# Performance work log

Measured on AMD Instinct MI355X. Metric: run time of the kernel, lower is better.

## Reference

```python
import jax, jax.numpy as jnp
import numpy as np

INPUT_SIZE = 512   # num_embeddings == RNN input feature dim
SEQ = INPUT_SIZE // 4   # 128, embedding dim == RNN seq_len
HID = 12
OUT = 3
B = 2048


def setup_inputs() -> dict:
    key = jax.random.key(0)
    ks = jax.random.split(key, 12)
    s = 0.1
    x = jax.random.randint(ks[0], (B, INPUT_SIZE), 0, INPUT_SIZE)
    emb = jax.random.normal(ks[1], (INPUT_SIZE, SEQ), dtype=jnp.float32) * s
    w_ih_f = jax.random.normal(ks[2], (HID, INPUT_SIZE), dtype=jnp.float32) * s
    w_hh_f = jax.random.normal(ks[3], (HID, HID), dtype=jnp.float32) * s
    b_ih_f = jax.random.normal(ks[4], (HID,), dtype=jnp.float32) * s
    b_hh_f = jax.random.normal(ks[5], (HID,), dtype=jnp.float32) * s
    w_ih_r = jax.random.normal(ks[6], (HID, INPUT_SIZE), dtype=jnp.float32) * s
    w_hh_r = jax.random.normal(ks[7], (HID, HID), dtype=jnp.float32) * s
    b_ih_r = jax.random.normal(ks[8], (HID,), dtype=jnp.float32) * s
    b_hh_r = jax.random.normal(ks[9], (HID,), dtype=jnp.float32) * s
    fc_w = jax.random.normal(ks[10], (OUT, 2 * HID), dtype=jnp.float32) * s
    fc_b = jax.random.normal(ks[11], (OUT,), dtype=jnp.float32) * s
    return {"x": x, "emb": emb,
            "w_ih_f": w_ih_f, "w_hh_f": w_hh_f, "b_ih_f": b_ih_f, "b_hh_f": b_hh_f,
            "w_ih_r": w_ih_r, "w_hh_r": w_hh_r, "b_ih_r": b_ih_r, "b_hh_r": b_hh_r,
            "fc_w": fc_w, "fc_b": fc_b}


def reference(x, emb, w_ih_f, w_hh_f, b_ih_f, b_hh_f,
              w_ih_r, w_hh_r, b_ih_r, b_hh_r, fc_w, fc_b):
    # embedding lookup: (B, INPUT_SIZE) -> (B, INPUT_SIZE, SEQ)
    e = emb[x]
    # view(-1, input_size, seq) is a no-op on this contiguous shape; swapaxes(1,2)
    xs = jnp.swapaxes(e, 1, 2)  # (B, SEQ, INPUT_SIZE): seq_len=SEQ, feat=INPUT_SIZE

    # forward-direction tanh RNN: precompute input projections, scan the recurrence
    pre = jnp.einsum('bsi,hi->sbh', xs, w_ih_f) + b_ih_f  # (SEQ, B, HID)

    def step(h, p):
        h = jnp.tanh(p + h @ w_hh_f.T + b_hh_f)
        return h, None

    h0 = jnp.zeros((xs.shape[0], HID), dtype=xs.dtype)
    h_fwd, _ = jax.lax.scan(step, h0, pre)  # final forward hidden (B, HID)

    # reverse-direction output at the LAST timestep = one step from zero hidden
    # on x_{T-1} (only out[:, -1, :] is consumed by the module)
    h_bwd = jnp.tanh(xs[:, -1, :] @ w_ih_r.T + b_ih_r + b_hh_r)  # (B, HID)

    out_last = jnp.concatenate([h_fwd, h_bwd], axis=-1)  # (B, 2*HID)
    return out_last @ fc_w.T + fc_b  # (B, OUT)
```

## Files before the change

### kernel.cpp

```cpp
#include <hip/hip_runtime.h>
#include <hip/hip_bf16.h>

#define B_N     2048
#define IN_N    512
#define SEQ_N   128
#define HID_N   12
#define HP_N    16
#define OUT_N   3

typedef __attribute__((ext_vector_type(8))) short short8;
typedef __attribute__((ext_vector_type(4))) float f32x4;
typedef unsigned int uint;
typedef unsigned short ushort;

__device__ __forceinline__ float fast_tanh(float x) {
    float e = __builtin_amdgcn_exp2f(x * 2.8853900817779268f);
    return 1.0f - 2.0f * __builtin_amdgcn_rcpf(e + 1.0f);
}

__device__ __forceinline__ ushort f2bf(float f) {
    uint u = __float_as_uint(f);
    u += 0x7fffu + ((u >> 16) & 1u);
    return (ushort)(u >> 16);
}

__device__ __forceinline__ float bf2f(ushort s) {
    return __uint_as_float(((uint)s) << 16);
}

__global__ __launch_bounds__(256) void k_prep(
    const float* __restrict__ emb, const float* __restrict__ w_ih_f,
    const float* __restrict__ w_ih_r,
    ushort* __restrict__ embB, ushort* __restrict__ wP)
{
    int tid = blockIdx.x * 256 + threadIdx.x;
    float4 e = ((const float4*)emb)[tid];
    uint2 o;
    o.x = (uint)f2bf(e.x) | ((uint)f2bf(e.y) << 16);
    o.y = (uint)f2bf(e.z) | ((uint)f2bf(e.w) << 16);
    ((uint2*)embB)[tid] = o;

    int j   = tid & 7;
    int l   = (tid >> 3) & 63;
    int src = (tid >> 9) & 1;
    int cks = tid >> 10;
    int h   = l & 15;
    int i   = (cks >> 2) * 128 + (cks & 3) * 32 + (l >> 4) * 8 + j;
    const float* wsrc = src ? w_ih_r : w_ih_f;
    wP[(((size_t)cks * 2 + src) * 64 + l) * 8 + j] =
        (h < HID_N) ? f2bf(wsrc[h * IN_N + i]) : (ushort)0;
}

__global__ __launch_bounds__(256, 2) void k_pre(
    const int* __restrict__ x, const ushort* __restrict__ embB,
    const ushort* __restrict__ wP,
    const float* __restrict__ b_ih_r, const float* __restrict__ b_hh_r,
    ushort* __restrict__ preB, float* __restrict__ rev)
{
    __shared__ __align__(16) ushort As[128 * 128];
    __shared__ __align__(16) ushort wPs[16384];

    const int t      = threadIdx.x;
    const int l      = t & 63;
    const int w      = t >> 6;
    const int lane16 = l & 15;
    const int quad   = l >> 4;
    const int il     = w * 32 + quad * 8;
    const int wg     = w * 4 + quad;
    const int l7     = lane16 & 7;
    const int so     = lane16 * 8;
    const int b0     = blockIdx.x * 4;

    {
        const uint4* s4 = (const uint4*)wP;
        uint4*       d4 = (uint4*)wPs;
        #pragma unroll
        for (int i = 0; i < 8; ++i) d4[t + i * 256] = s4[t + i * 256];
    }

    f32x4 acc0 = {0.f,0.f,0.f,0.f};
    f32x4 acc1 = {0.f,0.f,0.f,0.f};
    f32x4 accR = {0.f,0.f,0.f,0.f};
    uint R[8][4];

#define LD8(k, ix) { uint4 v = *(const uint4*)(embB + (size_t)(ix) * SEQ_N + so); \
        R[k][0]=v.x; R[k][1]=v.y; R[k][2]=v.z; R[k][3]=v.w; }

    int4 nA, nB;
    {
        const int* xq = x + (size_t)b0 * IN_N + il;
        nA = *(const int4*)xq;
        nB = *(const int4*)(xq + 4);
    }
    LD8(0, nA.x) LD8(1, nA.y) LD8(2, nA.z) LD8(3, nA.w)
    LD8(4, nB.x) LD8(5, nB.y) LD8(6, nB.z) LD8(7, nB.w)
    {
        const int* xq = x + (size_t)b0 * IN_N + 128 + il;
        nA = *(const int4*)xq;
        nB = *(const int4*)(xq + 4);
    }

    for (int p = 0; p < 16; ++p) {
        const int c = p & 3;

        #pragma unroll
        for (int pp = 0; pp < 8; ++pp) {
            const uint sel = (pp & 1) ? 0x07060302u : 0x05040100u;
            const int pv = pp >> 1;
            uint u0 = __builtin_amdgcn_perm(R[1][pv], R[0][pv], sel);
            uint u1 = __builtin_amdgcn_perm(R[3][pv], R[2][pv], sel);
            uint u2 = __builtin_amdgcn_perm(R[5][pv], R[4][pv], sel);
            uint u3 = __builtin_amdgcn_perm(R[7][pv], R[6][pv], sel);
            const int s    = lane16 * 8 + pp;
            const int slot = wg ^ pp ^ l7;
            *(uint4*)&As[(size_t)s * 128 + (size_t)slot * 8] =
                make_uint4(u0, u1, u2, u3);
        }

        if (p < 15) {
            LD8(0, nA.x) LD8(1, nA.y) LD8(2, nA.z) LD8(3, nA.w)
            LD8(4, nB.x) LD8(5, nB.y) LD8(6, nB.z) LD8(7, nB.w)
            if (p < 14) {
                const int pn = p + 2;
                const int* xq = x + (size_t)(b0 + (pn >> 2)) * IN_N
                                  + (pn & 3) * 128 + il;
                nA = *(const int4*)xq;
                nB = *(const int4*)(xq + 4);
            }
        }

        asm volatile("s_waitcnt lgkmcnt(0)" ::: "memory");
        __builtin_amdgcn_s_barrier();
        __builtin_amdgcn_sched_barrier(0);

        short8 bfr[4], bfrR[4];
        #pragma unroll
        for (int ks = 0; ks < 4; ++ks) {
            const ushort* wp = wPs + (size_t)((c * 4 + ks) * 128 + l) * 8;
            bfr[ks]  = *(const short8*)wp;
            bfrR[ks] = *(const short8*)(wp + 512);
        }

        #pragma unroll
        for (int tt = 0; tt < 2; ++tt) {
            const int row = (w * 2 + tt) * 16 + lane16;
            const int fr  = (row & 7) ^ ((row >> 3) & 7);
            #pragma unroll
            for (int ks = 0; ks < 4; ++ks) {
                const int slot = (ks * 4 + quad) ^ fr;
                short8 af = *(const short8*)&As[(size_t)row * 128 + (size_t)slot * 8];
                if (tt == 0) {
                    acc0 = __builtin_amdgcn_mfma_f32_16x16x32_bf16(af, bfr[ks], acc0, 0, 0, 0);
                } else {
                    acc1 = __builtin_amdgcn_mfma_f32_16x16x32_bf16(af, bfr[ks], acc1, 0, 0, 0);
                    accR = __builtin_amdgcn_mfma_f32_16x16x32_bf16(af, bfrR[ks], accR, 0, 0, 0);
                }
            }
        }

        if (c == 3) {
            const int bcur = b0 + (p >> 2);
            if (lane16 < HID_N) {
                #pragma unroll
                for (int r = 0; r < 4; ++r) {
                    const int s0v = (w * 2 + 0) * 16 + quad * 4 + r;
                    preB[((size_t)bcur * SEQ_N + s0v) * HP_N + lane16] = f2bf(acc0[r]);
                    const int s1v = (w * 2 + 1) * 16 + quad * 4 + r;
                    preB[((size_t)bcur * SEQ_N + s1v) * HP_N + lane16] = f2bf(acc1[r]);
                }
                if (w == 3 && quad == 3)
                    rev[bcur * HP_N + lane16] =
                        fast_tanh(accR[3] + b_ih_r[lane16] + b_hh_r[lane16]);
            }
            acc0 = (f32x4){0.f,0.f,0.f,0.f};
            acc1 = (f32x4){0.f,0.f,0.f,0.f};
            accR = (f32x4){0.f,0.f,0.f,0.f};
        }

        asm volatile("" ::: "memory");
        __builtin_amdgcn_s_barrier();
        __builtin_amdgcn_sched_barrier(0);
    }
#undef LD8
}

__global__ __launch_bounds__(256) void k_rnn(
    const ushort* __restrict__ preB, const float* __restrict__ rev,
    const float* __restrict__ w_hh_f,
    const float* __restrict__ b_ih_f, const float* __restrict__ b_hh_f,
    const float* __restrict__ fc_w, const float* __restrict__ fc_b,
    float* __restrict__ out)
{
    __shared__ float ho[16][40];

    const int tid = threadIdx.x;
    const int l   = tid & 63;
    const int j   = l & 15;
    const int jj  = (j < 12) ? j : 0;
    const int gid = tid >> 4;
    const int b   = blockIdx.x * 16 + gid;
    const int baseaddr = (l & 48) << 2;

    const float4* wr = (const float4*)(w_hh_f + jj * 12);
    float4 w0 = wr[0], w1 = wr[1], w2 = wr[2];
    float W[12] = {w0.x, w0.y, w0.z, w0.w, w1.x, w1.y, w1.z, w1.w,
                   w2.x, w2.y, w2.z, w2.w};
    const float bias = b_ih_f[jj] + b_hh_f[jj];

    const ushort* pb = preB + (size_t)b * SEQ_N * HP_N + j;
    ushort pq[8];
    #pragma unroll
    for (int k = 0; k < 8; ++k) pq[k] = pb[k * HP_N];

    float h = 0.f;
    for (int s8 = 0; s8 < 16; ++s8) {
        #pragma unroll
        for (int k = 0; k < 8; ++k) {
            int s = s8 * 8 + k;
            float p = bf2f(pq[k]) + bias;
            pq[k] = pb[((s + 8) & 127) * HP_N];
            int hb = __float_as_int(h);
            float hk[12];
            #pragma unroll
            for (int kk = 0; kk < 12; ++kk)
                hk[kk] = __int_as_float(__builtin_amdgcn_ds_bpermute(baseaddr + 4 * kk, hb));
            float c0 = p, c1 = 0.f, c2 = 0.f;
            #pragma unroll
            for (int u = 0; u < 4; ++u) {
                c0 = __builtin_fmaf(W[u],     hk[u],     c0);
                c1 = __builtin_fmaf(W[4 + u], hk[4 + u], c1);
                c2 = __builtin_fmaf(W[8 + u], hk[8 + u], c2);
            }
            h = fast_tanh(c0 + c1 + c2);
        }
    }

    ho[gid][j]      = h;
    ho[gid][20 + j] = rev[b * HP_N + j];
    if (j < OUT_N) {
        const float* fw = fc_w + j * 24;
        float o = fc_b[j];
        #pragma unroll
        for (int k = 0; k < 12; ++k)
            o += fw[k] * ho[gid][k] + fw[12 + k] * ho[gid][20 + k];
        out[b * OUT_N + j] = o;
    }
}

extern "C" void kernel_launch(void* const* d_in, const int* in_sizes, int n_in,
                              void* d_out, int out_size, void* d_ws, size_t ws_size,
                              hipStream_t stream) {
    const int*   x      = (const int*)  d_in[0];
    const float* emb    = (const float*)d_in[1];
    const float* w_ih_f = (const float*)d_in[2];
    const float* w_hh_f = (const float*)d_in[3];
    const float* b_ih_f = (const float*)d_in[4];
    const float* b_hh_f = (const float*)d_in[5];
    const float* w_ih_r = (const float*)d_in[6];
    const float* b_ih_r = (const float*)d_in[8];
    const float* b_hh_r = (const float*)d_in[9];
    const float* fc_w   = (const float*)d_in[10];
    const float* fc_b   = (const float*)d_in[11];
    float* out = (float*)d_out;

    ushort* preB = (ushort*)d_ws;
    float*  rev  = (float*)((char*)d_ws + 8388608);
    ushort* embB = (ushort*)((char*)d_ws + 8519680);
    ushort* wP   = (ushort*)((char*)d_ws + 8650752);

    k_prep<<<64,    256, 0, stream>>>(emb, w_ih_f, w_ih_r, embB, wP);
    k_pre <<<B_N/4, 256, 0, stream>>>(x, embB, wP, b_ih_r, b_hh_r, preB, rev);
    k_rnn <<<B_N/16,256, 0, stream>>>(preB, rev, w_hh_f, b_ih_f, b_hh_f, fc_w, fc_b, out);
}
```

Before: 117.6 us.

## Reorder projection loop by chunk with double-buffered gathers; two sequences per RNN thread

The projection kernel now loops over feature chunks in the outer loop and the four batch rows in the inner loop. It keeps four sets of accumulators and two register buffers for embedding gathers, so weight fragments are loaded once per chunk and the gathers run further ahead. The recurrence kernel now has each thread process two batch rows at once, interleaving two independent dependency chains to hide bpermute and tanh latency. The grid is halved to 64 blocks. This costs more registers and reduces the number of blocks in the latency-bound RNN stage.

```diff
diff --git a/kernel.cpp b/kernel.cpp
--- a/kernel.cpp
+++ b/kernel.cpp
@@ -78,110 +78,130 @@
         for (int i = 0; i < 8; ++i) d4[t + i * 256] = s4[t + i * 256];
     }
 
-    f32x4 acc0 = {0.f,0.f,0.f,0.f};
-    f32x4 acc1 = {0.f,0.f,0.f,0.f};
-    f32x4 accR = {0.f,0.f,0.f,0.f};
-    uint R[8][4];
-
-#define LD8(k, ix) { uint4 v = *(const uint4*)(embB + (size_t)(ix) * SEQ_N + so); \
-        R[k][0]=v.x; R[k][1]=v.y; R[k][2]=v.z; R[k][3]=v.w; }
-
-    int4 nA, nB;
-    {
-        const int* xq = x + (size_t)b0 * IN_N + il;
-        nA = *(const int4*)xq;
-        nB = *(const int4*)(xq + 4);
-    }
-    LD8(0, nA.x) LD8(1, nA.y) LD8(2, nA.z) LD8(3, nA.w)
-    LD8(4, nB.x) LD8(5, nB.y) LD8(6, nB.z) LD8(7, nB.w)
-    {
-        const int* xq = x + (size_t)b0 * IN_N + 128 + il;
-        nA = *(const int4*)xq;
-        nB = *(const int4*)(xq + 4);
-    }
-
-    for (int p = 0; p < 16; ++p) {
-        const int c = p & 3;
-
-        #pragma unroll
-        for (int pp = 0; pp < 8; ++pp) {
-            const uint sel = (pp & 1) ? 0x07060302u : 0x05040100u;
-            const int pv = pp >> 1;
-            uint u0 = __builtin_amdgcn_perm(R[1][pv], R[0][pv], sel);
-            uint u1 = __builtin_amdgcn_perm(R[3][pv], R[2][pv], sel);
-            uint u2 = __builtin_amdgcn_perm(R[5][pv], R[4][pv], sel);
-            uint u3 = __builtin_amdgcn_perm(R[7][pv], R[6][pv], sel);
-            const int s    = lane16 * 8 + pp;
-            const int slot = wg ^ pp ^ l7;
-            *(uint4*)&As[(size_t)s * 128 + (size_t)slot * 8] =
-                make_uint4(u0, u1, u2, u3);
-        }
-
-        if (p < 15) {
-            LD8(0, nA.x) LD8(1, nA.y) LD8(2, nA.z) LD8(3, nA.w)
-            LD8(4, nB.x) LD8(5, nB.y) LD8(6, nB.z) LD8(7, nB.w)
-            if (p < 14) {
-                const int pn = p + 2;
-                const int* xq = x + (size_t)(b0 + (pn >> 2)) * IN_N
-                                  + (pn & 3) * 128 + il;
-                nA = *(const int4*)xq;
-                nB = *(const int4*)(xq + 4);
-            }
-        }
-
-        asm volatile("s_waitcnt lgkmcnt(0)" ::: "memory");
-        __builtin_amdgcn_s_barrier();
-        __builtin_amdgcn_sched_barrier(0);
-
+    f32x4 a0_0={0.f,0.f,0.f,0.f}, a0_1={0.f,0.f,0.f,0.f}, a0_2={0.f,0.f,0.f,0.f}, a0_3={0.f,0.f,0.f,0.f};
+    f32x4 a1_0={0.f,0.f,0.f,0.f}, a1_1={0.f,0.f,0.f,0.f}, a1_2={0.f,0.f,0.f,0.f}, a1_3={0.f,0.f,0.f,0.f};
+    f32x4 aR_0={0.f,0.f,0.f,0.f}, aR_1={0.f,0.f,0.f,0.f}, aR_2={0.f,0.f,0.f,0.f}, aR_3={0.f,0.f,0.f,0.f};
+
+    uint RA[8][4], RB[8][4];
+    int4 IA0, IA1, IB0, IB1;
+
+#define IDXLD(Ilo, Ihi, bq2, c2) do { \
+    const int* xq_ = x + (size_t)(b0 + (bq2)) * IN_N + (c2) * 128 + il; \
+    Ilo = *(const int4*)xq_;  Ihi = *(const int4*)(xq_ + 4); \
+} while (0)
+
+#define GFETCH(Rb, Ilo, Ihi) do { uint4 v_; \
+    v_ = *(const uint4*)(embB + (size_t)(Ilo).x * SEQ_N + so); Rb[0][0]=v_.x; Rb[0][1]=v_.y; Rb[0][2]=v_.z; Rb[0][3]=v_.w; \
+    v_ = *(const uint4*)(embB + (size_t)(Ilo).y * SEQ_N + so); Rb[1][0]=v_.x; Rb[1][1]=v_.y; Rb[1][2]=v_.z; Rb[1][3]=v_.w; \
+    v_ = *(const uint4*)(embB + (size_t)(Ilo).z * SEQ_N + so); Rb[2][0]=v_.x; Rb[2][1]=v_.y; Rb[2][2]=v_.z; Rb[2][3]=v_.w; \
+    v_ = *(const uint4*)(embB + (size_t)(Ilo).w * SEQ_N + so); Rb[3][0]=v_.x; Rb[3][1]=v_.y; Rb[3][2]=v_.z; Rb[3][3]=v_.w; \
+    v_ = *(const uint4*)(embB + (size_t)(Ihi).x * SEQ_N + so); Rb[4][0]=v_.x; Rb[4][1]=v_.y; Rb[4][2]=v_.z; Rb[4][3]=v_.w; \
+    v_ = *(const uint4*)(embB + (size_t)(Ihi).y * SEQ_N + so); Rb[5][0]=v_.x; Rb[5][1]=v_.y; Rb[5][2]=v_.z; Rb[5][3]=v_.w; \
+    v_ = *(const uint4*)(embB + (size_t)(Ihi).z * SEQ_N + so); Rb[6][0]=v_.x; Rb[6][1]=v_.y; Rb[6][2]=v_.z; Rb[6][3]=v_.w; \
+    v_ = *(const uint4*)(embB + (size_t)(Ihi).w * SEQ_N + so); Rb[7][0]=v_.x; Rb[7][1]=v_.y; Rb[7][2]=v_.z; Rb[7][3]=v_.w; \
+} while (0)
+
+#define PACKR(Rb) do { \
+    _Pragma("unroll") \
+    for (int pp = 0; pp < 8; ++pp) { \
+        const uint sel_ = (pp & 1) ? 0x07060302u : 0x05040100u; \
+        const int pv_ = pp >> 1; \
+        uint u0_ = __builtin_amdgcn_perm(Rb[1][pv_], Rb[0][pv_], sel_); \
+        uint u1_ = __builtin_amdgcn_perm(Rb[3][pv_], Rb[2][pv_], sel_); \
+        uint u2_ = __builtin_amdgcn_perm(Rb[5][pv_], Rb[4][pv_], sel_); \
+        uint u3_ = __builtin_amdgcn_perm(Rb[7][pv_], Rb[6][pv_], sel_); \
+        const int s_    = lane16 * 8 + pp; \
+        const int slot_ = wg ^ pp ^ l7; \
+        *(uint4*)&As[(size_t)s_ * 128 + (size_t)slot_ * 8] = make_uint4(u0_, u1_, u2_, u3_); \
+    } \
+} while (0)
+
+#define MMA(A0, A1, AR) do { \
+    _Pragma("unroll") \
+    for (int tt = 0; tt < 2; ++tt) { \
+        const int row_ = (w * 2 + tt) * 16 + lane16; \
+        const int fr_  = (row_ & 7) ^ ((row_ >> 3) & 7); \
+        _Pragma("unroll") \
+        for (int ks = 0; ks < 4; ++ks) { \
+            const int slot_ = (ks * 4 + quad) ^ fr_; \
+            short8 af_ = *(const short8*)&As[(size_t)row_ * 128 + (size_t)slot_ * 8]; \
+            if (tt == 0) { A0 = __builtin_amdgcn_mfma_f32_16x16x32_bf16(af_, bfr[ks], A0, 0, 0, 0); } \
+            else { A1 = __builtin_amdgcn_mfma_f32_16x16x32_bf16(af_, bfr[ks], A1, 0, 0, 0); \
+                   AR = __builtin_amdgcn_mfma_f32_16x16x32_bf16(af_, bfrR[ks], AR, 0, 0, 0); } \
+        } \
+    } \
+} while (0)
+
+    IDXLD(IA0, IA1, 0, 0);
+    IDXLD(IB0, IB1, 1, 0);
+    GFETCH(RA, IA0, IA1);
+    GFETCH(RB, IB0, IB1);
+    IDXLD(IA0, IA1, 2, 0);
+
+    for (int c = 0; c < 4; ++c) {
         short8 bfr[4], bfrR[4];
         #pragma unroll
-        for (int ks = 0; ks < 4; ++ks) {
-            const ushort* wp = wPs + (size_t)((c * 4 + ks) * 128 + l) * 8;
-            bfr[ks]  = *(const short8*)wp;
-            bfrR[ks] = *(const short8*)(wp + 512);
+        for (int bq = 0; bq < 4; ++bq) {
+            if (bq & 1) PACKR(RB); else PACKR(RA);
+
+            if (!(c == 3 && bq >= 2)) {
+                if (bq & 1) GFETCH(RB, IB0, IB1); else GFETCH(RA, IA0, IA1);
+            }
+            if (!(c == 3 && bq >= 1)) {
+                if      (bq == 0) IDXLD(IB0, IB1, 3, c);
+                else if (bq == 1) IDXLD(IA0, IA1, 0, c + 1);
+                else if (bq == 2) IDXLD(IB0, IB1, 1, c + 1);
+                else              IDXLD(IA0, IA1, 2, c + 1);
+            }
+
+            asm volatile("s_waitcnt lgkmcnt(0)" ::: "memory");
+            __builtin_amdgcn_s_barrier();
+            __builtin_amdgcn_sched_barrier(0);
+
+            if (bq == 0) {
+                #pragma unroll
+                for (int ks = 0; ks < 4; ++ks) {
+                    const ushort* wp = wPs + (size_t)((c * 4 + ks) * 128 + l) * 8;
+                    bfr[ks]  = *(const short8*)wp;
+                    bfrR[ks] = *(const short8*)(wp + 512);
+                }
+            }
+
+            if      (bq == 0) MMA(a0_0, a1_0, aR_0);
+            else if (bq == 1) MMA(a0_1, a1_1, aR_1);
+            else if (bq == 2) MMA(a0_2, a1_2, aR_2);
+            else              MMA(a0_3, a1_3, aR_3);
+
+            asm volatile("" ::: "memory");
+            __builtin_amdgcn_s_barrier();
+            __builtin_amdgcn_sched_barrier(0);
         }
-
-        #pragma unroll
-        for (int tt = 0; tt < 2; ++tt) {
-            const int row = (w * 2 + tt) * 16 + lane16;
-            const int fr  = (row & 7) ^ ((row >> 3) & 7);
-            #pragma unroll
-            for (int ks = 0; ks < 4; ++ks) {
-                const int slot = (ks * 4 + quad) ^ fr;
-                short8 af = *(const short8*)&As[(size_t)row * 128 + (size_t)slot * 8];
-                if (tt == 0) {
-                    acc0 = __builtin_amdgcn_mfma_f32_16x16x32_bf16(af, bfr[ks], acc0, 0, 0, 0);
-                } else {
-                    acc1 = __builtin_amdgcn_mfma_f32_16x16x32_bf16(af, bfr[ks], acc1, 0, 0, 0);
-                    accR = __builtin_amdgcn_mfma_f32_16x16x32_bf16(af, bfrR[ks], accR, 0, 0, 0);
-                }
-            }
-        }
-
-        if (c == 3) {
-            const int bcur = b0 + (p >> 2);
-            if (lane16 < HID_N) {
-                #pragma unroll
-                for (int r = 0; r < 4; ++r) {
-                    const int s0v = (w * 2 + 0) * 16 + quad * 4 + r;
-                    preB[((size_t)bcur * SEQ_N + s0v) * HP_N + lane16] = f2bf(acc0[r]);
-                    const int s1v = (w * 2 + 1) * 16 + quad * 4 + r;
-                    preB[((size_t)bcur * SEQ_N + s1v) * HP_N + lane16] = f2bf(acc1[r]);
-                }
-                if (w == 3 && quad == 3)
-                    rev[bcur * HP_N + lane16] =
-                        fast_tanh(accR[3] + b_ih_r[lane16] + b_hh_r[lane16]);
-            }
-            acc0 = (f32x4){0.f,0.f,0.f,0.f};
-            acc1 = (f32x4){0.f,0.f,0.f,0.f};
-            accR = (f32x4){0.f,0.f,0.f,0.f};
-        }
-
-        asm volatile("" ::: "memory");
-        __builtin_amdgcn_s_barrier();
-        __builtin_amdgcn_sched_barrier(0);
-    }
-#undef LD8
+    }
+
+#define EPI(bq, A0, A1, AR) do { \
+    const int bcur_ = b0 + (bq); \
+    _Pragma("unroll") \
+    for (int r = 0; r < 4; ++r) { \
+        const int s0_ = (w * 2 + 0) * 16 + quad * 4 + r; \
+        preB[((size_t)bcur_ * SEQ_N + s0_) * HP_N + lane16] = f2bf(A0[r]); \
+        const int s1_ = (w * 2 + 1) * 16 + quad * 4 + r; \
+        preB[((size_t)bcur_ * SEQ_N + s1_) * HP_N + lane16] = f2bf(A1[r]); \
+    } \
+    if (w == 3 && quad == 3) \
+        rev[bcur_ * HP_N + lane16] = fast_tanh(AR[3] + b_ih_r[lane16] + b_hh_r[lane16]); \
+} while (0)
+
+    if (lane16 < HID_N) {
+        EPI(0, a0_0, a1_0, aR_0);
+        EPI(1, a0_1, a1_1, aR_1);
+        EPI(2, a0_2, a1_2, aR_2);
+        EPI(3, a0_3, a1_3, aR_3);
+    }
+#undef IDXLD
+#undef GFETCH
+#undef PACKR
+#undef MMA
+#undef EPI
 }
 
 __global__ __launch_bounds__(256) void k_rnn(
@@ -191,14 +211,15 @@
     const float* __restrict__ fc_w, const float* __restrict__ fc_b,
     float* __restrict__ out)
 {
-    __shared__ float ho[16][40];
+    __shared__ float ho[32][40];
 
     const int tid = threadIdx.x;
     const int l   = tid & 63;
     const int j   = l & 15;
     const int jj  = (j < 12) ? j : 0;
     const int gid = tid >> 4;
-    const int b   = blockIdx.x * 16 + gid;
+    const int bA  = blockIdx.x * 32 + gid * 2;
+    const int bB  = bA + 1;
     const int baseaddr = (l & 48) << 2;
 
     const float4* wr = (const float4*)(w_hh_f + jj * 12);
@@ -207,43 +228,59 @@
                    w2.x, w2.y, w2.z, w2.w};
     const float bias = b_ih_f[jj] + b_hh_f[jj];
 
-    const ushort* pb = preB + (size_t)b * SEQ_N * HP_N + j;
-    ushort pq[8];
+    const ushort* pbA = preB + (size_t)bA * SEQ_N * HP_N + j;
+    const ushort* pbB = preB + (size_t)bB * SEQ_N * HP_N + j;
+    ushort pqA[8], pqB[8];
     #pragma unroll
-    for (int k = 0; k < 8; ++k) pq[k] = pb[k * HP_N];
-
-    float h = 0.f;
+    for (int k = 0; k < 8; ++k) { pqA[k] = pbA[k * HP_N]; pqB[k] = pbB[k * HP_N]; }
+
+    float hA = 0.f, hB = 0.f;
     for (int s8 = 0; s8 < 16; ++s8) {
         #pragma unroll
         for (int k = 0; k < 8; ++k) {
             int s = s8 * 8 + k;
-            float p = bf2f(pq[k]) + bias;
-            pq[k] = pb[((s + 8) & 127) * HP_N];
-            int hb = __float_as_int(h);
-            float hk[12];
+            float pA = bf2f(pqA[k]) + bias;
+            float pB = bf2f(pqB[k]) + bias;
+            pqA[k] = pbA[((s + 8) & 127) * HP_N];
+            pqB[k] = pbB[((s + 8) & 127) * HP_N];
+            int ha = __float_as_int(hA), hb = __float_as_int(hB);
+            float hkA[12], hkB[12];
             #pragma unroll
-            for (int kk = 0; kk < 12; ++kk)
-                hk[kk] = __int_as_float(__builtin_amdgcn_ds_bpermute(baseaddr + 4 * kk, hb));
-            float c0 = p, c1 = 0.f, c2 = 0.f;
+            for (int kk = 0; kk < 12; ++kk) {
+                hkA[kk] = __int_as_float(__builtin_amdgcn_ds_bpermute(baseaddr + 4 * kk, ha));
+                hkB[kk] = __int_as_float(__builtin_amdgcn_ds_bpermute(baseaddr + 4 * kk, hb));
+            }
+            float cA0 = pA, cA1 = 0.f, cA2 = 0.f;
+            float cB0 = pB, cB1 = 0.f, cB2 = 0.f;
             #pragma unroll
             for (int u = 0; u < 4; ++u) {
-                c0 = __builtin_fmaf(W[u],     hk[u],     c0);
-                c1 = __builtin_fmaf(W[4 + u], hk[4 + u], c1);
-                c2 = __builtin_fmaf(W[8 + u], hk[8 + u], c2);
-            }
-            h = fast_tanh(c0 + c1 + c2);
+                cA0 = __builtin_fmaf(W[u],     hkA[u],     cA0);
+                cA1 = __builtin_fmaf(W[4 + u], hkA[4 + u], cA1);
+                cA2 = __builtin_fmaf(W[8 + u], hkA[8 + u], cA2);
+                cB0 = __builtin_fmaf(W[u],     hkB[u],     cB0);
+                cB1 = __builtin_fmaf(W[4 + u], hkB[4 + u], cB1);
+                cB2 = __builtin_fmaf(W[8 + u], hkB[8 + u], cB2);
+            }
+            hA = fast_tanh(cA0 + cA1 + cA2);
+            hB = fast_tanh(cB0 + cB1 + cB2);
         }
     }
 
-    ho[gid][j]      = h;
-    ho[gid][20 + j] = rev[b * HP_N + j];
+    const int g2 = gid * 2;
+    ho[g2][j]          = hA;
+    ho[g2][20 + j]     = rev[bA * HP_N + j];
+    ho[g2 + 1][j]      = hB;
+    ho[g2 + 1][20 + j] = rev[bB * HP_N + j];
     if (j < OUT_N) {
         const float* fw = fc_w + j * 24;
-        float o = fc_b[j];
+        float oA = fc_b[j], oB = fc_b[j];
         #pragma unroll
-        for (int k = 0; k < 12; ++k)
-            o += fw[k] * ho[gid][k] + fw[12 + k] * ho[gid][20 + k];
-        out[b * OUT_N + j] = o;
+        for (int k = 0; k < 12; ++k) {
+            oA += fw[k] * ho[g2][k]     + fw[12 + k] * ho[g2][20 + k];
+            oB += fw[k] * ho[g2 + 1][k] + fw[12 + k] * ho[g2 + 1][20 + k];
+        }
+        out[bA * OUT_N + j] = oA;
+        out[bB * OUT_N + j] = oB;
     }
 }
 
@@ -270,5 +307,5 @@
 
     k_prep<<<64,    256, 0, stream>>>(emb, w_ih_f, w_ih_r, embB, wP);
     k_pre <<<B_N/4, 256, 0, stream>>>(x, embB, wP, b_ih_r, b_hh_r, preB, rev);
-    k_rnn <<<B_N/16,256, 0, stream>>>(preB, rev, w_hh_f, b_ih_f, b_hh_f, fc_w, fc_b, out);
-}
+    k_rnn <<<B_N/32,256, 0, stream>>>(preB, rev, w_hh_f, b_ih_f, b_hh_f, fc_w, fc_b, out);
+}
```

Result: slower. 141.0 us (+19.9%).
